# Performance work log

Hardware: AMD Instinct MI355X
Metric: run time of the kernel (lower is better)

## Reference

```python
import jax, jax.numpy as jnp
import numpy as np

V, E, H = 39, 512, 256  # vocab, emb_size, hidden_size (hard-coded in VQVAE)
B, T = 512, 128


def _p(key, shape, scale=0.05):
    return scale * jax.random.normal(key, shape, dtype=jnp.float32)


def setup_inputs() -> dict:
    key = jax.random.key(0)
    ks = jax.random.split(key, 24)
    inp = {}
    inp["input"] = jax.random.randint(ks[0], (B, T), 0, V)
    inp["src_emb_table"] = _p(ks[1], (V, E))
    inp["trg_emb_table"] = _p(ks[2], (V, E))
    # encoder bidirectional GRU (input E, hidden H), PyTorch layout (3H, in)/(3H, H)
    inp["enc_Wih_f"] = _p(ks[3], (3 * H, E)); inp["enc_Whh_f"] = _p(ks[4], (3 * H, H))
    inp["enc_bih_f"] = _p(ks[5], (3 * H,)); inp["enc_bhh_f"] = _p(ks[6], (3 * H,))
    inp["enc_Wih_b"] = _p(ks[7], (3 * H, E)); inp["enc_Whh_b"] = _p(ks[8], (3 * H, H))
    inp["enc_bih_b"] = _p(ks[9], (3 * H,)); inp["enc_bhh_b"] = _p(ks[10], (3 * H,))
    # bridge: Linear(2H -> H, bias=True)
    inp["bridge_W"] = _p(ks[11], (H, 2 * H)); inp["bridge_b"] = _p(ks[12], (H,))
    # Bahdanau attention: key (2H->H), query (H->H), energy (H->1), all bias-free
    inp["attn_Wk"] = _p(ks[13], (H, 2 * H))
    inp["attn_Wq"] = _p(ks[14], (H, H))
    inp["attn_We"] = _p(ks[15], (1, H))
    # decoder GRU (input E + 2H = 1024, hidden H)
    inp["dec_Wih"] = _p(ks[16], (3 * H, E + 2 * H)); inp["dec_Whh"] = _p(ks[17], (3 * H, H))
    inp["dec_bih"] = _p(ks[18], (3 * H,)); inp["dec_bhh"] = _p(ks[19], (3 * H,))
    # pre_output: Linear(H + 2H + E = 1280 -> H, bias=False)
    inp["pre_W"] = _p(ks[20], (H, H + 2 * H + E))
    # generator: Linear(H -> V, bias=False)
    inp["gen_W"] = _p(ks[21], (V, H))
    return inp


def gru_cell(x, h, Wih, Whh, bih, bhh):
    """PyTorch GRU cell: gates ordered [r, z, n]."""
    gi = x @ Wih.T + bih
    gh = h @ Whh.T + bhh
    ir, iz, inn = jnp.split(gi, 3, axis=-1)
    hr, hz, hn = jnp.split(gh, 3, axis=-1)
    r = jax.nn.sigmoid(ir + hr)
    z = jax.nn.sigmoid(iz + hz)
    n = jnp.tanh(inn + r * hn)
    return (1.0 - z) * n + z * h


def reference(input, src_emb_table, trg_emb_table,
              enc_Wih_f, enc_Whh_f, enc_bih_f, enc_bhh_f,
              enc_Wih_b, enc_Whh_b, enc_bih_b, enc_bhh_b,
              bridge_W, bridge_b, attn_Wk, attn_Wq, attn_We,
              dec_Wih, dec_Whh, dec_bih, dec_bhh, pre_W, gen_W):
    Bv, Tv = input.shape
    src_mask = input != 0                       # (B, T)
    trg = input[:, :-1]
    trg_y = input[:, 1:]

    # ---- Encoder: bidirectional GRU over full length (lengths == T) ----
    x = src_emb_table[input]                    # (B, T, E)
    xs = jnp.swapaxes(x, 0, 1)                  # (T, B, E)
    h0 = jnp.zeros((Bv, H), x.dtype)

    def step_f(h, xt):
        hn = gru_cell(xt, h, enc_Wih_f, enc_Whh_f, enc_bih_f, enc_bhh_f)
        return hn, hn

    def step_b(h, xt):
        hn = gru_cell(xt, h, enc_Wih_b, enc_Whh_b, enc_bih_b, enc_bhh_b)
        return hn, hn

    hf, out_f = jax.lax.scan(step_f, h0, xs)
    hb, out_b = jax.lax.scan(step_b, h0, xs[::-1])
    out_b = out_b[::-1]
    enc_out = jnp.swapaxes(jnp.concatenate([out_f, out_b], -1), 0, 1)  # (B, T, 2H)
    enc_final = jnp.concatenate([hf, hb], -1)                          # (B, 2H)

    # ---- Decoder init + precomputed attention keys ----
    hidden = jnp.tanh(enc_final @ bridge_W.T + bridge_b)               # (B, H)
    proj_key = enc_out @ attn_Wk.T                                     # (B, T, H)

    te = jnp.swapaxes(trg_emb_table[trg], 0, 1)                        # (T-1, B, E)
    neg = jnp.finfo(x.dtype).min

    def dec_step(h, prev_embed):
        q = h @ attn_Wq.T                                              # (B, H)
        e = jnp.tanh(q[:, None, :] + proj_key) @ attn_We[0]            # (B, T)
        e = jnp.where(src_mask, e, neg)
        a = jax.nn.softmax(e, axis=-1)                                 # (B, T)
        ctx = jnp.einsum('bt,btd->bd', a, enc_out)                     # (B, 2H)
        hn = gru_cell(jnp.concatenate([prev_embed, ctx], -1), h,
                      dec_Wih, dec_Whh, dec_bih, dec_bhh)              # (B, H)
        # dropout p=0.2 is identity in eval mode
        pre = jnp.concatenate([prev_embed, hn, ctx], -1) @ pre_W.T     # (B, H)
        return hn, pre

    _, pres = jax.lax.scan(dec_step, hidden, te)                       # (T-1, B, H)

    # ---- Generator + NLL loss (sum, ignore_index=0) ----
    logp = jax.nn.log_softmax(pres @ gen_W.T, axis=-1)                 # (T-1, B, V)
    ty = jnp.swapaxes(trg_y, 0, 1)                                     # (T-1, B)
    nll = -jnp.take_along_axis(logp, ty[..., None], axis=-1)[..., 0]
    loss = jnp.sum(jnp.where(ty != 0, nll, 0.0))
    return loss
```

## Files before the change

kernel.cpp:

```cpp
#include <hip/hip_runtime.h>

#define BB 512
#define TT 128
#define EE 512
#define HH 256
#define VV 39
#define H3 768
#define H2 512
#define TM1 127
#define NEGF (-3.402823466e38f)

typedef unsigned short u16;
typedef unsigned int u32;
typedef __attribute__((ext_vector_type(8))) short s16x8;
typedef __attribute__((ext_vector_type(4))) float f32x4;
typedef __attribute__((ext_vector_type(2))) unsigned int u32x2;
typedef __attribute__((ext_vector_type(4))) unsigned int u32x4;

__device__ __forceinline__ float b2f(u16 u){ u32 x=((u32)u)<<16; return __uint_as_float(x); }
__device__ __forceinline__ u16 f2b(float f){ u32 x=__float_as_uint(f); u32 r=(x+0x7fffu+((x>>16)&1u))>>16; return (u16)r; }
__device__ __forceinline__ float sigm(float x){ return 1.f/(1.f+__expf(-x)); }
__device__ __forceinline__ float tanh1(float x){ float t=__expf(2.f*x); return 1.f-2.f/(t+1.f); }
__device__ __forceinline__ float bfl(u32 u){ return __uint_as_float(u<<16); }
__device__ __forceinline__ float bfh(u32 u){ return __uint_as_float(u & 0xffff0000u); }

#define MFMA __builtin_amdgcn_mfma_f32_16x16x32_bf16

__device__ __forceinline__ u32 aload(const u32* p){
  return __hip_atomic_load(p, __ATOMIC_RELAXED, __HIP_MEMORY_SCOPE_AGENT);
}
__device__ __forceinline__ void astore(u32* p, u32 v){
  __hip_atomic_store(p, v, __ATOMIC_RELAXED, __HIP_MEMORY_SCOPE_AGENT);
}
#define QF(g) ((g)*16)

__global__ __launch_bounds__(256) void k_tables(
    const float* __restrict__ src_emb, const float* __restrict__ trg_emb,
    const float* __restrict__ Wih_f, const float* __restrict__ bih_f,
    const float* __restrict__ Wih_b, const float* __restrict__ bih_b,
    const float* __restrict__ dec_Wih, const float* __restrict__ dec_bih,
    const float* __restrict__ pre_W,
    float* __restrict__ tab_gi_f, float* __restrict__ tab_gi_b,
    float* __restrict__ tab_dec, float* __restrict__ tab_pre)
{
  int v = blockIdx.x;
  int y = blockIdx.y;
  int tid = threadIdx.x;
  if (y < 9){
    int seg = y/3, part = y%3;
    int n = part*256 + tid;
    const float* emb; const float* W; const float* bias; float* out; int ldw;
    if (seg==0){ emb=src_emb; W=Wih_f; bias=bih_f; out=tab_gi_f; ldw=EE; }
    else if (seg==1){ emb=src_emb; W=Wih_b; bias=bih_b; out=tab_gi_b; ldw=EE; }
    else { emb=trg_emb; W=dec_Wih; bias=dec_bih; out=tab_dec; ldw=EE+H2; }
    float acc = bias[n];
    const float* er = emb + (size_t)v*EE;
    const float* wr = W + (size_t)n*ldw;
    for (int k=0;k<EE;k++) acc += er[k]*wr[k];
    out[(size_t)v*H3 + n] = acc;
  } else {
    int n = tid;
    float acc = 0.f;
    const float* er = trg_emb + (size_t)v*EE;
    const float* wr = pre_W + (size_t)n*1280;
    for (int k=0;k<EE;k++) acc += er[k]*wr[k];
    tab_pre[(size_t)v*HH + n] = acc;
  }
}

__global__ __launch_bounds__(256) void k_cvt_all(
    const float* __restrict__ eWhh_f, const float* __restrict__ eWhh_b,
    const float* __restrict__ dWhh, const float* __restrict__ dWih,
    const float* __restrict__ Wk, const float* __restrict__ Wq,
    const float* __restrict__ preW, const float* __restrict__ genW,
    u16* __restrict__ o1, u16* __restrict__ o2, u16* __restrict__ o3,
    u16* __restrict__ o4, u16* __restrict__ o5, u16* __restrict__ o6,
    u16* __restrict__ o7, u16* __restrict__ o8, u16* __restrict__ o9)
{
  int idx = blockIdx.x*256 + threadIdx.x;
  const float* src; u16* dst; int cols, ld, off, rel;
  if      (idx <  196608){ rel=idx;          src=eWhh_f; dst=o1; cols=256; ld=256;  off=0;   }
  else if (idx <  393216){ rel=idx-196608;   src=eWhh_b; dst=o2; cols=256; ld=256;  off=0;   }
  else if (idx <  589824){ rel=idx-393216;   src=dWhh;   dst=o3; cols=256; ld=256;  off=0;   }
  else if (idx <  983040){ rel=idx-589824;   src=dWih;   dst=o4; cols=512; ld=1024; off=512; }
  else if (idx < 1114112){ rel=idx-983040;   src=Wk;     dst=o5; cols=512; ld=512;  off=0;   }
  else if (idx < 1179648){ rel=idx-1114112;  src=Wq;     dst=o6; cols=256; ld=256;  off=0;   }
  else if (idx < 1245184){ rel=idx-1179648;  src=preW;   dst=o7; cols=256; ld=1280; off=512; }
  else if (idx < 1376256){ rel=idx-1245184;  src=preW;   dst=o8; cols=512; ld=1280; off=768; }
  else if (idx < 1392640){
    rel=idx-1376256; int r=rel>>8, c2=rel&255;
    o9[rel] = (r<VV)? f2b(genW[(size_t)r*HH + c2]) : (u16)0;
    return;
  }
  else return;
  int r = rel/cols, c2 = rel - r*cols;
  dst[rel] = f2b(src[(size_t)r*ld + off + c2]);
}

__global__ __launch_bounds__(512) void k_enc_all(const int* __restrict__ input,
    const u16* __restrict__ wb_f, const u16* __restrict__ wb_b,
    const float* __restrict__ bhh_f, const float* __restrict__ bhh_b,
    const float* __restrict__ tab_f, const float* __restrict__ tab_b,
    float* __restrict__ h_f, float* __restrict__ h_b, u16* __restrict__ enc_out)
{
  __shared__ float gh[8][772];
  __shared__ u16 hs[16][264];
  int bx = blockIdx.x;
  int dirb = bx>>6, mt = bx&63;
  int m0 = mt*8;
  int tid = threadIdx.x;
  const float* tab = dirb? tab_b : tab_f;
  const float* bhh = dirb? bhh_b : bhh_f;
  const u16* Wb = dirb? wb_b : wb_f;
  int c = tid & 255, rh = tid>>8;
  float b_r=bhh[c], b_z=bhh[c+256], b_n=bhh[c+512];
  float hreg[4];
  #pragma unroll
  for (int r=0;r<4;r++) hreg[r]=0.f;
  int wv = tid>>6, lane = tid&63, l15 = lane&15, kg=(lane>>4)*8;
  int n0w = wv*96;
  float* hOut = dirb? h_b : h_f;
  { u16* z = &hs[0][0]; for (int e=tid; e<16*264; e+=512) z[e]=0; }
  __syncthreads();

  for (int s=1; s<=TT; s++){
    int tcol = dirb? (TT-s) : (s-1);
    #pragma unroll
    for (int r=0;r<4;r++){
      int row = rh*4 + r;
      int b = m0 + row;
      int tok = input[b*TT + tcol];
      const float* tg = tab + (size_t)tok*H3;
      float g0=0.f, g1=0.f, g2=0.f;
      if (s>1){ g0=gh[row][c]; g1=gh[row][c+256]; g2=gh[row][c+512]; }
      float rg = sigm(tg[c]     + g0 + b_r);
      float zg = sigm(tg[c+256] + g1 + b_z);
      float ng = tanh1(tg[c+512] + rg*(g2 + b_n));
      float hv = (1.f-zg)*ng + zg*hreg[r];
      hreg[r] = hv;
      u16 hb = f2b(hv);
      hs[row][c] = hb;
      enc_out[((size_t)b*TT + tcol)*H2 + (size_t)dirb*HH + c] = hb;
    }
    if (s==TT){
      #pragma unroll
      for (int r=0;r<4;r++)
        hOut[(size_t)(m0+rh*4+r)*HH + c] = hreg[r];
      break;
    }
    __syncthreads();
    f32x4 acc[6];
    #pragma unroll
    for (int nt=0;nt<6;nt++) acc[nt]=(f32x4){0.f,0.f,0.f,0.f};
    const u16* ar0 = &hs[l15][0];
    s16x8 bcur[6], bnext[6];
    #pragma unroll
    for (int nt=0;nt<6;nt++)
      bcur[nt] = *(const s16x8*)(Wb + (size_t)(n0w+nt*16+l15)*HH + kg);
    #pragma unroll
    for (int ko=0;ko<256;ko+=32){
      if (ko<224){
        #pragma unroll
        for (int nt=0;nt<6;nt++)
          bnext[nt] = *(const s16x8*)(Wb + (size_t)(n0w+nt*16+l15)*HH + ko+32 + kg);
      }
      s16x8 a0 = *(const s16x8*)(ar0 + ko + kg);
      #pragma unroll
      for (int nt=0;nt<6;nt++)
        acc[nt] = MFMA(a0, bcur[nt], acc[nt], 0,0,0);
      #pragma unroll
      for (int nt=0;nt<6;nt++) bcur[nt]=bnext[nt];
    }
    int q4 = (lane>>4)*4;
    if (q4 < 8){
      #pragma unroll
      for (int nt=0;nt<6;nt++){
        int col = n0w + nt*16 + l15;
        #pragma unroll
        for (int j=0;j<4;j++)
          gh[q4 + j][col] = acc[nt][j];
      }
    }
    __syncthreads();
  }
}

__global__ __launch_bounds__(256) void k_proj(const u16* __restrict__ enc,
    const u16* __restrict__ W, u16* __restrict__ out, int nTot)
{
  int m0 = blockIdx.x*64;
  int tid = threadIdx.x, wv = tid>>6, lane = tid&63;
  int l15 = lane&15, kg = (lane>>4)*8;
  int n0 = blockIdx.y*256 + wv*64;
  f32x4 acc[4][4];
  #pragma unroll
  for (int rt=0;rt<4;rt++)
    #pragma unroll
    for (int nt=0;nt<4;nt++) acc[rt][nt] = (f32x4){0.f,0.f,0.f,0.f};
  for (int ko=0; ko<512; ko+=32){
    s16x8 a[4], b[4];
    #pragma unroll
    for (int rt=0;rt<4;rt++) a[rt] = *(const s16x8*)(enc + (size_t)(m0+rt*16+l15)*H2 + ko + kg);
    #pragma unroll
    for (int nt=0;nt<4;nt++) b[nt] = *(const s16x8*)(W + (size_t)(n0+nt*16+l15)*H2 + ko + kg);
    #pragma unroll
    for (int rt=0;rt<4;rt++)
      #pragma unroll
      for (int nt=0;nt<4;nt++)
        acc[rt][nt] = MFMA(a[rt], b[nt], acc[rt][nt], 0,0,0);
  }
  #pragma unroll
  for (int rt=0;rt<4;rt++){
    int rbase = m0 + rt*16 + (lane>>4)*4;
    #pragma unroll
    for (int nt=0;nt<4;nt++){
      int col = n0 + nt*16 + l15;
      #pragma unroll
      for (int j=0;j<4;j++)
        out[(size_t)(rbase+j)*nTot + col] = f2b(acc[rt][nt][j]);
    }
  }
}

__global__ __launch_bounds__(256) void k_bridge(const float* __restrict__ h_f,
    const float* __restrict__ h_b, const float* __restrict__ bw,
    const float* __restrict__ bb, float* __restrict__ hst)
{
  __shared__ float As[32][68];
  __shared__ float Ws[32][68];
  int n0=blockIdx.x*64, m0=blockIdx.y*64, tid=threadIdx.x;
  int ar=tid>>2, ak=(tid&3)*8;
  int rt=tid>>4, ct=tid&15;
  float acc[4][4];
  #pragma unroll
  for (int j=0;j<4;j++){
    #pragma unroll
    for (int l=0;l<4;l++) acc[j][l]=0.f;
  }
  for (int ko=0;ko<512;ko+=32){
    int k0=ko+ak;
    const float* asrc = (k0<256)? (h_f + (size_t)(m0+ar)*HH + k0)
                                : (h_b + (size_t)(m0+ar)*HH + (k0-256));
    float4 a0=*(const float4*)asrc, a1=*(const float4*)(asrc+4);
    const float* wsrc = bw + (size_t)(n0+ar)*H2 + k0;
    float4 w0=*(const float4*)wsrc, w1=*(const float4*)(wsrc+4);
    __syncthreads();
    As[ak+0][ar]=a0.x; As[ak+1][ar]=a0.y; As[ak+2][ar]=a0.z; As[ak+3][ar]=a0.w;
    As[ak+4][ar]=a1.x; As[ak+5][ar]=a1.y; As[ak+6][ar]=a1.z; As[ak+7][ar]=a1.w;
    Ws[ak+0][ar]=w0.x; Ws[ak+1][ar]=w0.y; Ws[ak+2][ar]=w0.z; Ws[ak+3][ar]=w0.w;
    Ws[ak+4][ar]=w1.x; Ws[ak+5][ar]=w1.y; Ws[ak+6][ar]=w1.z; Ws[ak+7][ar]=w1.w;
    __syncthreads();
    #pragma unroll
    for (int kk=0;kk<32;kk++){
      float4 a=*(const float4*)&As[kk][rt*4];
      float4 w=*(const float4*)&Ws[kk][ct*4];
      float a4[4]={a.x,a.y,a.z,a.w};
      float w4[4]={w.x,w.y,w.z,w.w};
      #pragma unroll
      for (int j=0;j<4;j++){
        #pragma unroll
        for (int l=0;l<4;l++) acc[j][l]+=a4[j]*w4[l];
      }
    }
  }
  #pragma unroll
  for (int j=0;j<4;j++){
    int row=m0+rt*4+j;
    #pragma unroll
    for (int l=0;l<4;l++){
      int col=n0+ct*4+l;
      hst[(size_t)row*HH+col]=tanh1(acc[j][l]+bb[col]);
    }
  }
}

__global__ __launch_bounds__(256) void k_boot(
    const float* __restrict__ hst, const u16* __restrict__ whh,
    const u16* __restrict__ wq, float* __restrict__ ghg,
    float* __restrict__ qg, float* __restrict__ nll)
{
  __shared__ u16 hsb[16][264];
  int bx=blockIdx.x, tid=threadIdx.x;
  int wv=tid>>6, lane=tid&63, l15=lane&15, kg=(lane>>4)*8;
  int b0=bx*16;
  {
    int c=tid;
    for (int r=0;r<16;r++) hsb[r][c] = f2b(hst[(size_t)(b0+r)*HH + c]);
  }
  if (tid<16) nll[b0+tid] = 0.f;
  __syncthreads();
  int rr = (lane>>4)*4;
  for (int nt=0;nt<12;nt++){
    int n0 = wv*192 + nt*16;
    f32x4 acc = (f32x4){0.f,0.f,0.f,0.f};
    for (int ko=0;ko<256;ko+=32){
      s16x8 a = *(const s16x8*)&hsb[l15][ko+kg];
      s16x8 bf = *(const s16x8*)(whh + (size_t)(n0+l15)*HH + ko + kg);
      acc = MFMA(a, bf, acc, 0,0,0);
    }
    #pragma unroll
    for (int jr=0;jr<4;jr++)
      ghg[(size_t)(b0+rr+jr)*H3 + n0 + l15] = acc[jr];
  }
  #pragma unroll
  for (int nt=0;nt<4;nt++){
    int n0 = wv*64 + nt*16;
    f32x4 acc = (f32x4){0.f,0.f,0.f,0.f};
    for (int ko=0;ko<256;ko+=32){
      s16x8 a = *(const s16x8*)&hsb[l15][ko+kg];
      s16x8 bf = *(const s16x8*)(wq + (size_t)(n0+l15)*HH + ko + kg);
      acc = MFMA(a, bf, acc, 0,0,0);
    }
    #pragma unroll
    for (int jr=0;jr<4;jr++)
      qg[(size_t)(b0+rr+jr)*HH + n0 + l15] = acc[jr];
  }
}

__global__ __launch_bounds__(512,4) void k_step(int L,
    const int* __restrict__ input,
    const float* __restrict__ tab_dec, const float* __restrict__ tab_pre,
    const float* __restrict__ bhh, const float* __restrict__ We,
    const u16* __restrict__ whh, const u16* __restrict__ wq,
    const u16* __restrict__ wph, const u16* __restrict__ wgen,
    const u16* __restrict__ pk, const u16* __restrict__ eih,
    const u16* __restrict__ epc,
    float* __restrict__ hst, u32* __restrict__ qgu, float* __restrict__ ghg,
    u16* __restrict__ gicW, const u16* __restrict__ gicR,
    u16* __restrict__ pcW, const u16* __restrict__ pcR,
    float* __restrict__ nll, u32* __restrict__ fl)
{
  __shared__ __align__(16) char smem[54400];
  u16 (*gicL)[776] = (u16(*)[776])smem;
  u16 (*pcl)[264]  = (u16(*)[264])(smem+24832);
  u16 (*hsb)[264]  = (u16(*)[264])(smem+33280);
  u16 (*preb)[264] = (u16(*)[264])(smem+41728);
  float (*lgt)[64] = (float(*)[64])(smem+50176);
  int* stokL       = (int*)(smem+54272);
  float* aL  = (float*)smem;
  int* stok  = (int*)(smem+512);
  float* qS  = (float*)(smem+1024);
  float (*pG)[768] = (float(*)[768])(smem+2048);
  float (*pP)[256] = (float(*)[256])(smem+26624);

  int bx=blockIdx.x, tid=threadIdx.x;
  int wv=tid>>6, lane=tid&63, l15=lane&15, kg=(lane>>4)*8;

  if (bx < 32 && L > 0){
    int s = L-1;
    int b0 = bx*16;
    int rr = (lane>>4)*4;
    float b_r, b_z, b_n;
    { int c=tid&255; b_r=bhh[c]; b_z=bhh[c+256]; b_n=bhh[c+512]; }
    for (int idx=tid; idx<1536; idx+=512){
      int r=idx/96, cc=(idx%96)*8;
      *(u32x4*)&gicL[r][cc] = *(const u32x4*)(gicR + (size_t)(b0+r)*H3 + cc);
    }
    { int r=tid>>5, cc=(tid&31)*8;
      *(u32x4*)&pcl[r][cc] = *(const u32x4*)(pcR + (size_t)(b0+r)*HH + cc); }
    if (tid<16) stokL[tid] = input[(b0+tid)*TT + s];
    __syncthreads();
    {
      int c = tid&255, rh = tid>>8;
      for (int r=rh*8; r<rh*8+8; r++){
        int bb = b0+r;
        const float* tg = tab_dec + (size_t)stokL[r]*H3;
        const float* gr = ghg + (size_t)bb*H3;
        float rg = sigm(tg[c]     + b2f(gicL[r][c])     + gr[c]     + b_r);
        float zg = sigm(tg[c+256] + b2f(gicL[r][c+256]) + gr[c+256] + b_z);
        float ng = tanh1(tg[c+512] + b2f(gicL[r][c+512]) + rg*(gr[c+512] + b_n));
        float hv = (1.f-zg)*ng + zg*hst[(size_t)bb*HH + c];
        hst[(size_t)bb*HH + c] = hv;
        hsb[r][c] = f2b(hv);
      }
    }
    __syncthreads();
    {
      f32x4 accq[2];
      accq[0]=(f32x4){0.f,0.f,0.f,0.f}; accq[1]=(f32x4){0.f,0.f,0.f,0.f};
      #pragma unroll
      for (int ko=0;ko<256;ko+=32){
        s16x8 bq0 = *(const s16x8*)(wq + (size_t)(wv*32+l15)*HH + ko + kg);
        s16x8 bq1 = *(const s16x8*)(wq + (size_t)(wv*32+16+l15)*HH + ko + kg);
        s16x8 a = *(const s16x8*)&hsb[l15][ko+kg];
        accq[0] = MFMA(a,bq0,accq[0],0,0,0);
        accq[1] = MFMA(a,bq1,accq[1],0,0,0);
      }
      #pragma unroll
      for (int nt=0;nt<2;nt++)
        #pragma unroll
        for (int jr=0;jr<4;jr++)
          astore(qgu + (size_t)(b0+rr+jr)*HH + wv*32+nt*16+l15,
                 __float_as_uint(accq[nt][jr]));
    }
    __syncthreads();
    if (tid==0) astore(&fl[QF(bx)], (u32)L);
    {
      f32x4 acc6[6];
      #pragma unroll
      for (int nt=0;nt<6;nt++) acc6[nt]=(f32x4){0.f,0.f,0.f,0.f};
      #pragma unroll
      for (int ko=0;ko<256;ko+=32){
        s16x8 b6[6];
        #pragma unroll
        for (int nt=0;nt<6;nt++)
          b6[nt] = *(const s16x8*)(whh + (size_t)(wv*96+nt*16+l15)*HH + ko + kg);
        s16x8 a = *(const s16x8*)&hsb[l15][ko+kg];
        #pragma unroll
        for (int nt=0;nt<6;nt++) acc6[nt]=MFMA(a,b6[nt],acc6[nt],0,0,0);
      }
      #pragma unroll
      for (int nt=0;nt<6;nt++)
        #pragma unroll
        for (int jr=0;jr<4;jr++)
          ghg[(size_t)(b0+rr+jr)*H3 + wv*96+nt*16+l15] = acc6[nt][jr];
    }
    {
      f32x4 accp[2];
      accp[0]=(f32x4){0.f,0.f,0.f,0.f}; accp[1]=(f32x4){0.f,0.f,0.f,0.f};
      #pragma unroll
      for (int ko=0;ko<256;ko+=32){
        s16x8 bp0 = *(const s16x8*)(wph + (size_t)(wv*32+l15)*HH + ko + kg);
        s16x8 bp1 = *(const s16x8*)(wph + (size_t)(wv*32+16+l15)*HH + ko + kg);
        s16x8 a = *(const s16x8*)&hsb[l15][ko+kg];
        accp[0] = MFMA(a,bp0,accp[0],0,0,0);
        accp[1] = MFMA(a,bp1,accp[1],0,0,0);
      }
      #pragma unroll
      for (int nt=0;nt<2;nt++)
        #pragma unroll
        for (int jr=0;jr<4;jr++){
          int r = rr+jr, col = wv*32+nt*16+l15;
          float pv = accp[nt][jr] + b2f(pcl[r][col]) + tab_pre[(size_t)stokL[r]*HH + col];
          preb[r][col] = f2b(pv);
        }
    }
    __syncthreads();
    if (wv<4){
      int n0 = wv*16;
      f32x4 acc = (f32x4){0.f,0.f,0.f,0.f};
      for (int ko=0;ko<256;ko+=32){
        s16x8 a = *(const s16x8*)&preb[l15][ko+kg];
        s16x8 bf = *(const s16x8*)(wgen + (size_t)(n0+l15)*HH + ko + kg);
        acc = MFMA(a,bf,acc,0,0,0);
      }
      #pragma unroll
      for (int jr=0;jr<4;jr++) lgt[rr+jr][n0+l15] = acc[jr];
    }
    __syncthreads();
    {
      int r = wv*4 + (lane>>4);
      if (r < 16){
        float v0 = lgt[r][l15];
        float v1 = lgt[r][l15+16];
        float v2 = (l15<7)? lgt[r][l15+32] : NEGF;
        float m = fmaxf(fmaxf(v0,v1),v2);
        #pragma unroll
        for (int off=8; off; off>>=1) m = fmaxf(m, __shfl_xor(m,off));
        float pe = __expf(v0-m) + __expf(v1-m) + ((l15<7)? __expf(v2-m) : 0.f);
        #pragma unroll
        for (int off=8; off; off>>=1) pe += __shfl_xor(pe,off);
        if (l15==0){
          int ty = input[(b0+r)*TT + s+1];
          if (ty != 0) nll[b0+r] += m + __logf(pe) - lgt[r][ty];
        }
      }
    }
    __syncthreads();
  }

  if (L < TM1){
    int r2 = bx;
    int g2 = r2>>4;
    int l32 = lane&31;
    if (tid < TT) stok[tid] = input[r2*TT + tid];
    const u16* pkb = pk + (size_t)r2*TT*HH + l32*8;
    s16x8 kv[8];
    #pragma unroll
    for (int it=0; it<8; it++){
      int t = wv*16 + it*2 + (lane>>5);
      kv[it] = *(const s16x8*)(pkb + (size_t)t*HH);
    }
    float4 w0 = *(const float4*)(We + l32*8);
    float4 w1 = *(const float4*)(We + l32*8 + 4);
    __syncthreads();
    if (L > 0){
      if (tid==0){
        while (aload(&fl[QF(g2)]) < (u32)L) __builtin_amdgcn_s_sleep(1);
      }
      __syncthreads();
    }
    if (tid < 256) qS[tid] = __uint_as_float(aload(qgu + (size_t)r2*HH + tid));
    __syncthreads();
    float4 q0 = *(const float4*)&qS[l32*8];
    float4 q1 = *(const float4*)&qS[l32*8 + 4];
    #pragma unroll
    for (int it=0; it<8; it++){
      int t = wv*16 + it*2 + (lane>>5);
      s16x8 k8 = kv[it];
      float sE = tanh1(q0.x + b2f((u16)k8[0]))*w0.x
               + tanh1(q0.y + b2f((u16)k8[1]))*w0.y
               + tanh1(q0.z + b2f((u16)k8[2]))*w0.z
               + tanh1(q0.w + b2f((u16)k8[3]))*w0.w
               + tanh1(q1.x + b2f((u16)k8[4]))*w1.x
               + tanh1(q1.y + b2f((u16)k8[5]))*w1.y
               + tanh1(q1.z + b2f((u16)k8[6]))*w1.z
               + tanh1(q1.w + b2f((u16)k8[7]))*w1.w;
      #pragma unroll
      for (int off=16; off; off>>=1) sE += __shfl_xor(sE, off);
      if (l32==0) aL[t] = stok[t] ? sE : NEGF;
    }
    __syncthreads();
    if (wv==0){
      float v0 = aL[lane], v1 = aL[64+lane];
      float m = fmaxf(v0,v1);
      #pragma unroll
      for (int off=32; off; off>>=1) m = fmaxf(m, __shfl_xor(m,off));
      float p0 = __expf(v0-m), p1 = __expf(v1-m);
      float sS = p0+p1;
      #pragma unroll
      for (int off=32; off; off>>=1) sS += __shfl_xor(sS,off);
      float inv = 1.f/sS;
      aL[lane] = p0*inv; aL[64+lane] = p1*inv;
    }
    __syncthreads();
    {
      float gA[8], gB[4], pA[4];
      #pragma unroll
      for (int e=0;e<8;e++) gA[e]=0.f;
      #pragma unroll
      for (int e=0;e<4;e++){ gB[e]=0.f; pA[e]=0.f; }
      const u16* ei = eih + (size_t)r2*TT*H3;
      const u16* ep = epc + (size_t)r2*TT*HH;
      int t0 = wv*16;
      #pragma unroll 4
      for (int tt=0; tt<16; tt++){
        int t = t0+tt;
        float a = aL[t];
        u32x4 v0 = *(const u32x4*)(ei + (size_t)t*H3 + lane*8);
        u32x2 v1 = *(const u32x2*)(ei + (size_t)t*H3 + 512 + lane*4);
        u32x2 v2 = *(const u32x2*)(ep + (size_t)t*HH + lane*4);
        gA[0]+=a*bfl(v0.x); gA[1]+=a*bfh(v0.x);
        gA[2]+=a*bfl(v0.y); gA[3]+=a*bfh(v0.y);
        gA[4]+=a*bfl(v0.z); gA[5]+=a*bfh(v0.z);
        gA[6]+=a*bfl(v0.w); gA[7]+=a*bfh(v0.w);
        gB[0]+=a*bfl(v1.x); gB[1]+=a*bfh(v1.x);
        gB[2]+=a*bfl(v1.y); gB[3]+=a*bfh(v1.y);
        pA[0]+=a*bfl(v2.x); pA[1]+=a*bfh(v2.x);
        pA[2]+=a*bfl(v2.y); pA[3]+=a*bfh(v2.y);
      }
      #pragma unroll
      for (int e=0;e<8;e++) pG[wv][lane*8+e] = gA[e];
      #pragma unroll
      for (int e=0;e<4;e++) pG[wv][512+lane*4+e] = gB[e];
      #pragma unroll
      for (int e=0;e<4;e++) pP[wv][lane*4+e] = pA[e];
    }
    __syncthreads();
    {
      float sG = 0.f;
      #pragma unroll
      for (int w=0;w<8;w++) sG += pG[w][tid];
      gicW[(size_t)r2*H3 + tid] = f2b(sG);
      if (tid < 256){
        float sH = 0.f;
        #pragma unroll
        for (int w=0;w<8;w++) sH += pG[w][512+tid];
        gicW[(size_t)r2*H3 + 512 + tid] = f2b(sH);
      } else {
        int d = tid-256;
        float sP = 0.f;
        #pragma unroll
        for (int w=0;w<8;w++) sP += pP[w][d];
        pcW[(size_t)r2*HH + d] = f2b(sP);
      }
    }
  }
}

__global__ __launch_bounds__(256) void k_loss(const float* __restrict__ nll,
                                              float* __restrict__ out)
{
  __shared__ float sm[256];
  int tid=threadIdx.x;
  float s = nll[tid] + nll[tid+256];
  sm[tid]=s; __syncthreads();
  for (int off=128; off; off>>=1){
    if (tid<off) sm[tid]+=sm[tid+off];
    __syncthreads();
  }
  if (tid==0) out[0]=sm[0];
}

extern "C" void kernel_launch(void* const* d_in, const int* in_sizes, int n_in,
                              void* d_out, int out_size, void* d_ws, size_t ws_size,
                              hipStream_t stream)
{
  const int*   input    = (const int*)  d_in[0];
  const float* src_emb  = (const float*)d_in[1];
  const float* trg_emb  = (const float*)d_in[2];
  const float* eWih_f   = (const float*)d_in[3];
  const float* eWhh_f   = (const float*)d_in[4];
  const float* ebih_f   = (const float*)d_in[5];
  const float* ebhh_f   = (const float*)d_in[6];
  const float* eWih_b   = (const float*)d_in[7];
  const float* eWhh_b   = (const float*)d_in[8];
  const float* ebih_b   = (const float*)d_in[9];
  const float* ebhh_b   = (const float*)d_in[10];
  const float* bridge_W = (const float*)d_in[11];
  const float* bridge_b = (const float*)d_in[12];
  const float* attn_Wk  = (const float*)d_in[13];
  const float* attn_Wq  = (const float*)d_in[14];
  const float* attn_We  = (const float*)d_in[15];
  const float* dec_Wih  = (const float*)d_in[16];
  const float* dec_Whh  = (const float*)d_in[17];
  const float* dec_bih  = (const float*)d_in[18];
  const float* dec_bhh  = (const float*)d_in[19];
  const float* pre_W    = (const float*)d_in[20];
  const float* gen_W    = (const float*)d_in[21];

  float* F = (float*)d_ws;
  size_t o=0;
  u32* fl         = (u32*)(F+o); o+=2048;
  float* tab_gi_f = F+o; o+=(size_t)VV*H3;
  float* tab_gi_b = F+o; o+=(size_t)VV*H3;
  float* tab_dec  = F+o; o+=(size_t)VV*H3;
  float* tab_pre  = F+o; o+=(size_t)VV*HH;
  float* h_f      = F+o; o+=(size_t)BB*HH;
  float* h_b      = F+o; o+=(size_t)BB*HH;
  float* hst      = F+o; o+=(size_t)BB*HH;
  float* qg       = F+o; o+=(size_t)BB*HH;
  float* ghg      = F+o; o+=(size_t)BB*H3;
  float* nll      = F+o; o+=(size_t)BB;
  u16* U = (u16*)(F+o);
  size_t uo=0;
  u16* enc_out = U+uo; uo+=(size_t)BB*TT*H2;
  u16* pk      = U+uo; uo+=(size_t)BB*TT*HH;
  u16* eih     = U+uo; uo+=(size_t)BB*TT*H3;
  u16* epc     = U+uo; uo+=(size_t)BB*TT*HH;
  u16* gic0    = U+uo; uo+=(size_t)BB*H3;
  u16* gic1    = U+uo; uo+=(size_t)BB*H3;
  u16* pc0     = U+uo; uo+=(size_t)BB*HH;
  u16* pc1     = U+uo; uo+=(size_t)BB*HH;
  u16* wb_ehh_f= U+uo; uo+=(size_t)H3*HH;
  u16* wb_ehh_b= U+uo; uo+=(size_t)H3*HH;
  u16* wb_dhh  = U+uo; uo+=(size_t)H3*HH;
  u16* wb_dih  = U+uo; uo+=(size_t)H3*H2;
  u16* wb_wk   = U+uo; uo+=(size_t)HH*H2;
  u16* wb_wq   = U+uo; uo+=(size_t)HH*HH;
  u16* wb_ph   = U+uo; uo+=(size_t)HH*HH;
  u16* wb_pc   = U+uo; uo+=(size_t)HH*H2;
  u16* wb_gen  = U+uo; uo+=(size_t)64*HH;

  dim3 blk(256,1,1);
  k_tables<<<dim3(VV,10),blk,0,stream>>>(src_emb,trg_emb,eWih_f,ebih_f,eWih_b,ebih_b,
                                         dec_Wih,dec_bih,pre_W,
                                         tab_gi_f,tab_gi_b,tab_dec,tab_pre);
  k_cvt_all<<<dim3(5440),blk,0,stream>>>(eWhh_f,eWhh_b,dec_Whh,dec_Wih,attn_Wk,attn_Wq,pre_W,gen_W,
                                         wb_ehh_f,wb_ehh_b,wb_dhh,wb_dih,wb_wk,wb_wq,
                                         wb_ph,wb_pc,wb_gen);
  k_enc_all<<<dim3(128),dim3(512),0,stream>>>(input,wb_ehh_f,wb_ehh_b,ebhh_f,ebhh_b,
                                              tab_gi_f,tab_gi_b,h_f,h_b,enc_out);
  k_proj<<<dim3(1024,1),blk,0,stream>>>(enc_out,wb_wk,pk,HH);
  k_proj<<<dim3(1024,3),blk,0,stream>>>(enc_out,wb_dih,eih,H3);
  k_proj<<<dim3(1024,1),blk,0,stream>>>(enc_out,wb_pc,epc,HH);
  k_bridge<<<dim3(4,8),blk,0,stream>>>(h_f,h_b,bridge_W,bridge_b,hst);
  k_boot<<<dim3(32),blk,0,stream>>>(hst,wb_dhh,wb_wq,ghg,qg,nll);
  hipMemsetAsync(fl, 0, 8192, stream);

  for (int L=0; L<=TM1; L++){
    u16* gw = (L&1)? gic1 : gic0;
    u16* gr = (L&1)? gic0 : gic1;
    u16* pw = (L&1)? pc1 : pc0;
    u16* pr = (L&1)? pc0 : pc1;
    k_step<<<dim3(512),dim3(512),0,stream>>>(L,input,tab_dec,tab_pre,dec_bhh,attn_We,
                                             wb_dhh,wb_wq,wb_ph,wb_gen,
                                             pk,eih,epc,hst,(u32*)qg,ghg,
                                             gw,gr,pw,pr,nll,fl);
  }
  k_loss<<<dim3(1),blk,0,stream>>>(nll,(float*)d_out);
}
```

Baseline: 8.778 ms.

## Fuse decoder steps into one persistent kernel with flag-based inter-block sync

Replaces the 128 per-step k_step launches with a single persistent kernel of 256 blocks that loops over all decoder steps. Blocks exchange gate and pre-output contributions through double-buffered global buffers, using atomic flags and spin-waits in place of kernel boundaries. Each attention block now handles two batch rows instead of one, and the encoder is split into 256 blocks of 4 rows to raise parallelism. This removes launch overhead and implicit grid barriers, but adds spin-wait latency and relies on all 256 blocks being co-resident to avoid deadlock.

```diff
diff --git a/kernel.cpp b/kernel.cpp
--- a/kernel.cpp
+++ b/kernel.cpp
@@ -33,6 +33,7 @@
   __hip_atomic_store(p, v, __ATOMIC_RELAXED, __HIP_MEMORY_SCOPE_AGENT);
 }
 #define QF(g) ((g)*16)
+#define GF(b) (512 + (b)*16)
 
 __global__ __launch_bounds__(256) void k_tables(
     const float* __restrict__ src_emb, const float* __restrict__ trg_emb,
@@ -103,20 +104,19 @@
     const float* __restrict__ tab_f, const float* __restrict__ tab_b,
     float* __restrict__ h_f, float* __restrict__ h_b, u16* __restrict__ enc_out)
 {
-  __shared__ float gh[8][772];
+  __shared__ float gh[4][772];
   __shared__ u16 hs[16][264];
   int bx = blockIdx.x;
-  int dirb = bx>>6, mt = bx&63;
-  int m0 = mt*8;
+  int dirb = bx>>7, mt = bx&127;
+  int m0 = mt*4;
   int tid = threadIdx.x;
   const float* tab = dirb? tab_b : tab_f;
   const float* bhh = dirb? bhh_b : bhh_f;
   const u16* Wb = dirb? wb_b : wb_f;
   int c = tid & 255, rh = tid>>8;
   float b_r=bhh[c], b_z=bhh[c+256], b_n=bhh[c+512];
-  float hreg[4];
-  #pragma unroll
-  for (int r=0;r<4;r++) hreg[r]=0.f;
+  float hreg[2];
+  hreg[0]=0.f; hreg[1]=0.f;
   int wv = tid>>6, lane = tid&63, l15 = lane&15, kg=(lane>>4)*8;
   int n0w = wv*96;
   float* hOut = dirb? h_b : h_f;
@@ -126,8 +126,8 @@
   for (int s=1; s<=TT; s++){
     int tcol = dirb? (TT-s) : (s-1);
     #pragma unroll
-    for (int r=0;r<4;r++){
-      int row = rh*4 + r;
+    for (int r=0;r<2;r++){
+      int row = rh*2 + r;
       int b = m0 + row;
       int tok = input[b*TT + tcol];
       const float* tg = tab + (size_t)tok*H3;
@@ -144,8 +144,8 @@
     }
     if (s==TT){
       #pragma unroll
-      for (int r=0;r<4;r++)
-        hOut[(size_t)(m0+rh*4+r)*HH + c] = hreg[r];
+      for (int r=0;r<2;r++)
+        hOut[(size_t)(m0+rh*2+r)*HH + c] = hreg[r];
       break;
     }
     __syncthreads();
@@ -172,13 +172,13 @@
       for (int nt=0;nt<6;nt++) bcur[nt]=bnext[nt];
     }
     int q4 = (lane>>4)*4;
-    if (q4 < 8){
+    if (q4 == 0){
       #pragma unroll
       for (int nt=0;nt<6;nt++){
         int col = n0w + nt*16 + l15;
         #pragma unroll
         for (int j=0;j<4;j++)
-          gh[q4 + j][col] = acc[nt][j];
+          gh[j][col] = acc[nt][j];
       }
     }
     __syncthreads();
@@ -317,7 +317,7 @@
   }
 }
 
-__global__ __launch_bounds__(512,4) void k_step(int L,
+__global__ __launch_bounds__(512,2) void k_dec_p(
     const int* __restrict__ input,
     const float* __restrict__ tab_dec, const float* __restrict__ tab_pre,
     const float* __restrict__ bhh, const float* __restrict__ We,
@@ -326,8 +326,7 @@
     const u16* __restrict__ pk, const u16* __restrict__ eih,
     const u16* __restrict__ epc,
     float* __restrict__ hst, u32* __restrict__ qgu, float* __restrict__ ghg,
-    u16* __restrict__ gicW, const u16* __restrict__ gicR,
-    u16* __restrict__ pcW, const u16* __restrict__ pcR,
+    u32* __restrict__ gp0, u32* __restrict__ gp1,
     float* __restrict__ nll, u32* __restrict__ fl)
 {
   __shared__ __align__(16) char smem[54400];
@@ -336,244 +335,252 @@
   u16 (*hsb)[264]  = (u16(*)[264])(smem+33280);
   u16 (*preb)[264] = (u16(*)[264])(smem+41728);
   float (*lgt)[64] = (float(*)[64])(smem+50176);
-  int* stokL       = (int*)(smem+54272);
   float* aL  = (float*)smem;
-  int* stok  = (int*)(smem+512);
   float* qS  = (float*)(smem+1024);
-  float (*pG)[768] = (float(*)[768])(smem+2048);
-  float (*pP)[256] = (float(*)[256])(smem+26624);
+  float (*pG)[768] = (float(*)[768])(smem+4096);
+  float (*pP)[256] = (float(*)[256])(smem+28672);
+  __shared__ int stokA[256];
+  __shared__ int stokG[16];
 
   int bx=blockIdx.x, tid=threadIdx.x;
   int wv=tid>>6, lane=tid&63, l15=lane&15, kg=(lane>>4)*8;
-
-  if (bx < 32 && L > 0){
-    int s = L-1;
-    int b0 = bx*16;
-    int rr = (lane>>4)*4;
-    float b_r, b_z, b_n;
-    { int c=tid&255; b_r=bhh[c]; b_z=bhh[c+256]; b_n=bhh[c+512]; }
-    for (int idx=tid; idx<1536; idx+=512){
-      int r=idx/96, cc=(idx%96)*8;
-      *(u32x4*)&gicL[r][cc] = *(const u32x4*)(gicR + (size_t)(b0+r)*H3 + cc);
-    }
-    { int r=tid>>5, cc=(tid&31)*8;
-      *(u32x4*)&pcl[r][cc] = *(const u32x4*)(pcR + (size_t)(b0+r)*HH + cc); }
-    if (tid<16) stokL[tid] = input[(b0+tid)*TT + s];
-    __syncthreads();
-    {
-      int c = tid&255, rh = tid>>8;
-      for (int r=rh*8; r<rh*8+8; r++){
-        int bb = b0+r;
-        const float* tg = tab_dec + (size_t)stokL[r]*H3;
-        const float* gr = ghg + (size_t)bb*H3;
-        float rg = sigm(tg[c]     + b2f(gicL[r][c])     + gr[c]     + b_r);
-        float zg = sigm(tg[c+256] + b2f(gicL[r][c+256]) + gr[c+256] + b_z);
-        float ng = tanh1(tg[c+512] + b2f(gicL[r][c+512]) + rg*(gr[c+512] + b_n));
-        float hv = (1.f-zg)*ng + zg*hst[(size_t)bb*HH + c];
-        hst[(size_t)bb*HH + c] = hv;
-        hsb[r][c] = f2b(hv);
-      }
-    }
-    __syncthreads();
-    {
-      f32x4 accq[2];
-      accq[0]=(f32x4){0.f,0.f,0.f,0.f}; accq[1]=(f32x4){0.f,0.f,0.f,0.f};
-      #pragma unroll
-      for (int ko=0;ko<256;ko+=32){
-        s16x8 bq0 = *(const s16x8*)(wq + (size_t)(wv*32+l15)*HH + ko + kg);
-        s16x8 bq1 = *(const s16x8*)(wq + (size_t)(wv*32+16+l15)*HH + ko + kg);
-        s16x8 a = *(const s16x8*)&hsb[l15][ko+kg];
-        accq[0] = MFMA(a,bq0,accq[0],0,0,0);
-        accq[1] = MFMA(a,bq1,accq[1],0,0,0);
-      }
-      #pragma unroll
-      for (int nt=0;nt<2;nt++)
-        #pragma unroll
-        for (int jr=0;jr<4;jr++)
-          astore(qgu + (size_t)(b0+rr+jr)*HH + wv*32+nt*16+l15,
-                 __float_as_uint(accq[nt][jr]));
-    }
-    __syncthreads();
-    if (tid==0) astore(&fl[QF(bx)], (u32)L);
-    {
-      f32x4 acc6[6];
-      #pragma unroll
-      for (int nt=0;nt<6;nt++) acc6[nt]=(f32x4){0.f,0.f,0.f,0.f};
-      #pragma unroll
-      for (int ko=0;ko<256;ko+=32){
-        s16x8 b6[6];
+  int rr = (lane>>4)*4;
+  int b0 = bx*16;
+  int rowA = bx*2;
+  int g2 = bx>>3;
+  int l32 = lane&31;
+  float b_r, b_z, b_n;
+  { int c=tid&255; b_r=bhh[c]; b_z=bhh[c+256]; b_n=bhh[c+512]; }
+  float4 w0 = *(const float4*)(We + l32*8);
+  float4 w1 = *(const float4*)(We + l32*8 + 4);
+  if (tid<256) stokA[tid] = input[(rowA + (tid>>7))*TT + (tid&127)];
+  __syncthreads();
+
+  for (int L=0; L<=TM1; L++){
+    if (bx < 32 && L > 0){
+      int s = L-1;
+      const u32* gpR = ((L-1)&1)? gp1 : gp0;
+      if (tid<8){
+        while (aload(&fl[GF(bx*8+tid)]) < (u32)L) __builtin_amdgcn_s_sleep(1);
+      }
+      if (tid<16) stokG[tid] = input[(b0+tid)*TT + s];
+      __syncthreads();
+      for (int idx=tid; idx<8192; idx+=512){
+        int r = idx>>9, k = idx&511;
+        u32 v = aload(gpR + (size_t)(b0+r)*512 + k);
+        if (k<384) *(u32*)&gicL[r][2*k] = v;
+        else       *(u32*)&pcl[r][2*(k-384)] = v;
+      }
+      __syncthreads();
+      {
+        int c = tid&255, rh = tid>>8;
+        for (int r=rh*8; r<rh*8+8; r++){
+          int bb = b0+r;
+          const float* tg = tab_dec + (size_t)stokG[r]*H3;
+          const float* gr = ghg + (size_t)bb*H3;
+          float rg = sigm(tg[c]     + b2f(gicL[r][c])     + gr[c]     + b_r);
+          float zg = sigm(tg[c+256] + b2f(gicL[r][c+256]) + gr[c+256] + b_z);
+          float ng = tanh1(tg[c+512] + b2f(gicL[r][c+512]) + rg*(gr[c+512] + b_n));
+          float hv = (1.f-zg)*ng + zg*hst[(size_t)bb*HH + c];
+          hst[(size_t)bb*HH + c] = hv;
+          hsb[r][c] = f2b(hv);
+        }
+      }
+      __syncthreads();
+      {
+        f32x4 accq[2];
+        accq[0]=(f32x4){0.f,0.f,0.f,0.f}; accq[1]=(f32x4){0.f,0.f,0.f,0.f};
+        #pragma unroll
+        for (int ko=0;ko<256;ko+=32){
+          s16x8 bq0 = *(const s16x8*)(wq + (size_t)(wv*32+l15)*HH + ko + kg);
+          s16x8 bq1 = *(const s16x8*)(wq + (size_t)(wv*32+16+l15)*HH + ko + kg);
+          s16x8 a = *(const s16x8*)&hsb[l15][ko+kg];
+          accq[0] = MFMA(a,bq0,accq[0],0,0,0);
+          accq[1] = MFMA(a,bq1,accq[1],0,0,0);
+        }
+        #pragma unroll
+        for (int nt=0;nt<2;nt++)
+          #pragma unroll
+          for (int jr=0;jr<4;jr++)
+            astore(qgu + (size_t)(b0+rr+jr)*HH + wv*32+nt*16+l15,
+                   __float_as_uint(accq[nt][jr]));
+      }
+      __syncthreads();
+      if (tid==0) astore(&fl[QF(bx)], (u32)L);
+      {
+        f32x4 acc6[6];
+        #pragma unroll
+        for (int nt=0;nt<6;nt++) acc6[nt]=(f32x4){0.f,0.f,0.f,0.f};
+        #pragma unroll
+        for (int ko=0;ko<256;ko+=32){
+          s16x8 b6[6];
+          #pragma unroll
+          for (int nt=0;nt<6;nt++)
+            b6[nt] = *(const s16x8*)(whh + (size_t)(wv*96+nt*16+l15)*HH + ko + kg);
+          s16x8 a = *(const s16x8*)&hsb[l15][ko+kg];
+          #pragma unroll
+          for (int nt=0;nt<6;nt++) acc6[nt]=MFMA(a,b6[nt],acc6[nt],0,0,0);
+        }
         #pragma unroll
         for (int nt=0;nt<6;nt++)
-          b6[nt] = *(const s16x8*)(whh + (size_t)(wv*96+nt*16+l15)*HH + ko + kg);
-        s16x8 a = *(const s16x8*)&hsb[l15][ko+kg];
-        #pragma unroll
-        for (int nt=0;nt<6;nt++) acc6[nt]=MFMA(a,b6[nt],acc6[nt],0,0,0);
-      }
-      #pragma unroll
-      for (int nt=0;nt<6;nt++)
-        #pragma unroll
-        for (int jr=0;jr<4;jr++)
-          ghg[(size_t)(b0+rr+jr)*H3 + wv*96+nt*16+l15] = acc6[nt][jr];
-    }
-    {
-      f32x4 accp[2];
-      accp[0]=(f32x4){0.f,0.f,0.f,0.f}; accp[1]=(f32x4){0.f,0.f,0.f,0.f};
-      #pragma unroll
-      for (int ko=0;ko<256;ko+=32){
-        s16x8 bp0 = *(const s16x8*)(wph + (size_t)(wv*32+l15)*HH + ko + kg);
-        s16x8 bp1 = *(const s16x8*)(wph + (size_t)(wv*32+16+l15)*HH + ko + kg);
-        s16x8 a = *(const s16x8*)&hsb[l15][ko+kg];
-        accp[0] = MFMA(a,bp0,accp[0],0,0,0);
-        accp[1] = MFMA(a,bp1,accp[1],0,0,0);
-      }
-      #pragma unroll
-      for (int nt=0;nt<2;nt++)
-        #pragma unroll
-        for (int jr=0;jr<4;jr++){
-          int r = rr+jr, col = wv*32+nt*16+l15;
-          float pv = accp[nt][jr] + b2f(pcl[r][col]) + tab_pre[(size_t)stokL[r]*HH + col];
-          preb[r][col] = f2b(pv);
-        }
-    }
-    __syncthreads();
-    if (wv<4){
-      int n0 = wv*16;
-      f32x4 acc = (f32x4){0.f,0.f,0.f,0.f};
-      for (int ko=0;ko<256;ko+=32){
-        s16x8 a = *(const s16x8*)&preb[l15][ko+kg];
-        s16x8 bf = *(const s16x8*)(wgen + (size_t)(n0+l15)*HH + ko + kg);
-        acc = MFMA(a,bf,acc,0,0,0);
-      }
-      #pragma unroll
-      for (int jr=0;jr<4;jr++) lgt[rr+jr][n0+l15] = acc[jr];
-    }
-    __syncthreads();
-    {
-      int r = wv*4 + (lane>>4);
-      if (r < 16){
-        float v0 = lgt[r][l15];
-        float v1 = lgt[r][l15+16];
-        float v2 = (l15<7)? lgt[r][l15+32] : NEGF;
-        float m = fmaxf(fmaxf(v0,v1),v2);
-        #pragma unroll
-        for (int off=8; off; off>>=1) m = fmaxf(m, __shfl_xor(m,off));
-        float pe = __expf(v0-m) + __expf(v1-m) + ((l15<7)? __expf(v2-m) : 0.f);
-        #pragma unroll
-        for (int off=8; off; off>>=1) pe += __shfl_xor(pe,off);
-        if (l15==0){
-          int ty = input[(b0+r)*TT + s+1];
-          if (ty != 0) nll[b0+r] += m + __logf(pe) - lgt[r][ty];
-        }
-      }
-    }
-    __syncthreads();
-  }
-
-  if (L < TM1){
-    int r2 = bx;
-    int g2 = r2>>4;
-    int l32 = lane&31;
-    if (tid < TT) stok[tid] = input[r2*TT + tid];
-    const u16* pkb = pk + (size_t)r2*TT*HH + l32*8;
-    s16x8 kv[8];
-    #pragma unroll
-    for (int it=0; it<8; it++){
-      int t = wv*16 + it*2 + (lane>>5);
-      kv[it] = *(const s16x8*)(pkb + (size_t)t*HH);
-    }
-    float4 w0 = *(const float4*)(We + l32*8);
-    float4 w1 = *(const float4*)(We + l32*8 + 4);
-    __syncthreads();
-    if (L > 0){
-      if (tid==0){
-        while (aload(&fl[QF(g2)]) < (u32)L) __builtin_amdgcn_s_sleep(1);
-      }
-      __syncthreads();
-    }
-    if (tid < 256) qS[tid] = __uint_as_float(aload(qgu + (size_t)r2*HH + tid));
-    __syncthreads();
-    float4 q0 = *(const float4*)&qS[l32*8];
-    float4 q1 = *(const float4*)&qS[l32*8 + 4];
-    #pragma unroll
-    for (int it=0; it<8; it++){
-      int t = wv*16 + it*2 + (lane>>5);
-      s16x8 k8 = kv[it];
-      float sE = tanh1(q0.x + b2f((u16)k8[0]))*w0.x
-               + tanh1(q0.y + b2f((u16)k8[1]))*w0.y
-               + tanh1(q0.z + b2f((u16)k8[2]))*w0.z
-               + tanh1(q0.w + b2f((u16)k8[3]))*w0.w
-               + tanh1(q1.x + b2f((u16)k8[4]))*w1.x
-               + tanh1(q1.y + b2f((u16)k8[5]))*w1.y
-               + tanh1(q1.z + b2f((u16)k8[6]))*w1.z
-               + tanh1(q1.w + b2f((u16)k8[7]))*w1.w;
-      #pragma unroll
-      for (int off=16; off; off>>=1) sE += __shfl_xor(sE, off);
-      if (l32==0) aL[t] = stok[t] ? sE : NEGF;
-    }
-    __syncthreads();
-    if (wv==0){
-      float v0 = aL[lane], v1 = aL[64+lane];
-      float m = fmaxf(v0,v1);
-      #pragma unroll
-      for (int off=32; off; off>>=1) m = fmaxf(m, __shfl_xor(m,off));
-      float p0 = __expf(v0-m), p1 = __expf(v1-m);
-      float sS = p0+p1;
-      #pragma unroll
-      for (int off=32; off; off>>=1) sS += __shfl_xor(sS,off);
-      float inv = 1.f/sS;
-      aL[lane] = p0*inv; aL[64+lane] = p1*inv;
-    }
-    __syncthreads();
-    {
-      float gA[8], gB[4], pA[4];
-      #pragma unroll
-      for (int e=0;e<8;e++) gA[e]=0.f;
-      #pragma unroll
-      for (int e=0;e<4;e++){ gB[e]=0.f; pA[e]=0.f; }
-      const u16* ei = eih + (size_t)r2*TT*H3;
-      const u16* ep = epc + (size_t)r2*TT*HH;
-      int t0 = wv*16;
-      #pragma unroll 4
-      for (int tt=0; tt<16; tt++){
-        int t = t0+tt;
-        float a = aL[t];
-        u32x4 v0 = *(const u32x4*)(ei + (size_t)t*H3 + lane*8);
-        u32x2 v1 = *(const u32x2*)(ei + (size_t)t*H3 + 512 + lane*4);
-        u32x2 v2 = *(const u32x2*)(ep + (size_t)t*HH + lane*4);
-        gA[0]+=a*bfl(v0.x); gA[1]+=a*bfh(v0.x);
-        gA[2]+=a*bfl(v0.y); gA[3]+=a*bfh(v0.y);
-        gA[4]+=a*bfl(v0.z); gA[5]+=a*bfh(v0.z);
-        gA[6]+=a*bfl(v0.w); gA[7]+=a*bfh(v0.w);
-        gB[0]+=a*bfl(v1.x); gB[1]+=a*bfh(v1.x);
-        gB[2]+=a*bfl(v1.y); gB[3]+=a*bfh(v1.y);
-        pA[0]+=a*bfl(v2.x); pA[1]+=a*bfh(v2.x);
-        pA[2]+=a*bfl(v2.y); pA[3]+=a*bfh(v2.y);
-      }
-      #pragma unroll
-      for (int e=0;e<8;e++) pG[wv][lane*8+e] = gA[e];
-      #pragma unroll
-      for (int e=0;e<4;e++) pG[wv][512+lane*4+e] = gB[e];
-      #pragma unroll
-      for (int e=0;e<4;e++) pP[wv][lane*4+e] = pA[e];
-    }
-    __syncthreads();
-    {
-      float sG = 0.f;
-      #pragma unroll
-      for (int w=0;w<8;w++) sG += pG[w][tid];
-      gicW[(size_t)r2*H3 + tid] = f2b(sG);
-      if (tid < 256){
-        float sH = 0.f;
-        #pragma unroll
-        for (int w=0;w<8;w++) sH += pG[w][512+tid];
-        gicW[(size_t)r2*H3 + 512 + tid] = f2b(sH);
-      } else {
-        int d = tid-256;
-        float sP = 0.f;
-        #pragma unroll
-        for (int w=0;w<8;w++) sP += pP[w][d];
-        pcW[(size_t)r2*HH + d] = f2b(sP);
-      }
+          #pragma unroll
+          for (int jr=0;jr<4;jr++)
+            ghg[(size_t)(b0+rr+jr)*H3 + wv*96+nt*16+l15] = acc6[nt][jr];
+      }
+      {
+        f32x4 accp[2];
+        accp[0]=(f32x4){0.f,0.f,0.f,0.f}; accp[1]=(f32x4){0.f,0.f,0.f,0.f};
+        #pragma unroll
+        for (int ko=0;ko<256;ko+=32){
+          s16x8 bp0 = *(const s16x8*)(wph + (size_t)(wv*32+l15)*HH + ko + kg);
+          s16x8 bp1 = *(const s16x8*)(wph + (size_t)(wv*32+16+l15)*HH + ko + kg);
+          s16x8 a = *(const s16x8*)&hsb[l15][ko+kg];
+          accp[0] = MFMA(a,bp0,accp[0],0,0,0);
+          accp[1] = MFMA(a,bp1,accp[1],0,0,0);
+        }
+        #pragma unroll
+        for (int nt=0;nt<2;nt++)
+          #pragma unroll
+          for (int jr=0;jr<4;jr++){
+            int r = rr+jr, col = wv*32+nt*16+l15;
+            float pv = accp[nt][jr] + b2f(pcl[r][col]) + tab_pre[(size_t)stokG[r]*HH + col];
+            preb[r][col] = f2b(pv);
+          }
+      }
+      __syncthreads();
+      if (wv<4){
+        int n0 = wv*16;
+        f32x4 acc = (f32x4){0.f,0.f,0.f,0.f};
+        for (int ko=0;ko<256;ko+=32){
+          s16x8 a = *(const s16x8*)&preb[l15][ko+kg];
+          s16x8 bf = *(const s16x8*)(wgen + (size_t)(n0+l15)*HH + ko + kg);
+          acc = MFMA(a,bf,acc,0,0,0);
+        }
+        #pragma unroll
+        for (int jr=0;jr<4;jr++) lgt[rr+jr][n0+l15] = acc[jr];
+      }
+      __syncthreads();
+      {
+        int r = wv*4 + (lane>>4);
+        if (r < 16){
+          float v0 = lgt[r][l15];
+          float v1 = lgt[r][l15+16];
+          float v2 = (l15<7)? lgt[r][l15+32] : NEGF;
+          float m = fmaxf(fmaxf(v0,v1),v2);
+          #pragma unroll
+          for (int off=8; off; off>>=1) m = fmaxf(m, __shfl_xor(m,off));
+          float pe = __expf(v0-m) + __expf(v1-m) + ((l15<7)? __expf(v2-m) : 0.f);
+          #pragma unroll
+          for (int off=8; off; off>>=1) pe += __shfl_xor(pe,off);
+          if (l15==0){
+            int ty = input[(b0+r)*TT + s+1];
+            if (ty != 0) nll[b0+r] += m + __logf(pe) - lgt[r][ty];
+          }
+        }
+      }
+      __syncthreads();
+    }
+
+    if (L < TM1){
+      u32* gpW = (L&1)? gp1 : gp0;
+      if (L > 0){
+        if (tid==0){
+          while (aload(&fl[QF(g2)]) < (u32)L) __builtin_amdgcn_s_sleep(1);
+        }
+        __syncthreads();
+      }
+      qS[tid] = __uint_as_float(aload(qgu + (size_t)rowA*HH + tid));
+      __syncthreads();
+      for (int rp=0; rp<2; rp++){
+        int row = rowA + rp;
+        const u16* pkb = pk + (size_t)row*TT*HH + l32*8;
+        s16x8 kv[8];
+        #pragma unroll
+        for (int it=0; it<8; it++){
+          int t = wv*16 + it*2 + (lane>>5);
+          kv[it] = *(const s16x8*)(pkb + (size_t)t*HH);
+        }
+        float4 q0 = *(const float4*)&qS[rp*256 + l32*8];
+        float4 q1 = *(const float4*)&qS[rp*256 + l32*8 + 4];
+        #pragma unroll
+        for (int it=0; it<8; it++){
+          int t = wv*16 + it*2 + (lane>>5);
+          s16x8 k8 = kv[it];
+          float sE = tanh1(q0.x + b2f((u16)k8[0]))*w0.x
+                   + tanh1(q0.y + b2f((u16)k8[1]))*w0.y
+                   + tanh1(q0.z + b2f((u16)k8[2]))*w0.z
+                   + tanh1(q0.w + b2f((u16)k8[3]))*w0.w
+                   + tanh1(q1.x + b2f((u16)k8[4]))*w1.x
+                   + tanh1(q1.y + b2f((u16)k8[5]))*w1.y
+                   + tanh1(q1.z + b2f((u16)k8[6]))*w1.z
+                   + tanh1(q1.w + b2f((u16)k8[7]))*w1.w;
+          #pragma unroll
+          for (int off=16; off; off>>=1) sE += __shfl_xor(sE, off);
+          if (l32==0) aL[t] = stokA[rp*128+t] ? sE : NEGF;
+        }
+        __syncthreads();
+        if (wv==0){
+          float v0 = aL[lane], v1 = aL[64+lane];
+          float m = fmaxf(v0,v1);
+          #pragma unroll
+          for (int off=32; off; off>>=1) m = fmaxf(m, __shfl_xor(m,off));
+          float p0 = __expf(v0-m), p1 = __expf(v1-m);
+          float sS = p0+p1;
+          #pragma unroll
+          for (int off=32; off; off>>=1) sS += __shfl_xor(sS,off);
+          float inv = 1.f/sS;
+          aL[lane] = p0*inv; aL[64+lane] = p1*inv;
+        }
+        __syncthreads();
+        {
+          float gA[8], gB[4], pA[4];
+          #pragma unroll
+          for (int e=0;e<8;e++) gA[e]=0.f;
+          #pragma unroll
+          for (int e=0;e<4;e++){ gB[e]=0.f; pA[e]=0.f; }
+          const u16* ei = eih + (size_t)row*TT*H3;
+          const u16* ep = epc + (size_t)row*TT*HH;
+          int t0 = wv*16;
+          #pragma unroll 4
+          for (int tt=0; tt<16; tt++){
+            int t = t0+tt;
+            float a = aL[t];
+            u32x4 v0 = *(const u32x4*)(ei + (size_t)t*H3 + lane*8);
+            u32x2 v1 = *(const u32x2*)(ei + (size_t)t*H3 + 512 + lane*4);
+            u32x2 v2 = *(const u32x2*)(ep + (size_t)t*HH + lane*4);
+            gA[0]+=a*bfl(v0.x); gA[1]+=a*bfh(v0.x);
+            gA[2]+=a*bfl(v0.y); gA[3]+=a*bfh(v0.y);
+            gA[4]+=a*bfl(v0.z); gA[5]+=a*bfh(v0.z);
+            gA[6]+=a*bfl(v0.w); gA[7]+=a*bfh(v0.w);
+            gB[0]+=a*bfl(v1.x); gB[1]+=a*bfh(v1.x);
+            gB[2]+=a*bfl(v1.y); gB[3]+=a*bfh(v1.y);
+            pA[0]+=a*bfl(v2.x); pA[1]+=a*bfh(v2.x);
+            pA[2]+=a*bfl(v2.y); pA[3]+=a*bfh(v2.y);
+          }
+          #pragma unroll
+          for (int e=0;e<8;e++) pG[wv][lane*8+e] = gA[e];
+          #pragma unroll
+          for (int e=0;e<4;e++) pG[wv][512+lane*4+e] = gB[e];
+          #pragma unroll
+          for (int e=0;e<4;e++) pP[wv][lane*4+e] = pA[e];
+        }
+        __syncthreads();
+        {
+          float lo=0.f, hi=0.f;
+          if (tid<384){
+            #pragma unroll
+            for (int w=0;w<8;w++){ lo += pG[w][2*tid]; hi += pG[w][2*tid+1]; }
+          } else {
+            int d = tid-384;
+            #pragma unroll
+            for (int w=0;w<8;w++){ lo += pP[w][2*d]; hi += pP[w][2*d+1]; }
+          }
+          u32 v = (u32)f2b(lo) | ((u32)f2b(hi)<<16);
+          astore(gpW + (size_t)row*512 + tid, v);
+        }
+        __syncthreads();
+      }
+      if (tid==0) astore(&fl[GF(bx)], (u32)(L+1));
     }
   }
 }
@@ -621,7 +628,7 @@
 
   float* F = (float*)d_ws;
   size_t o=0;
-  u32* fl         = (u32*)(F+o); o+=2048;
+  u32* fl         = (u32*)(F+o); o+=8192;
   float* tab_gi_f = F+o; o+=(size_t)VV*H3;
   float* tab_gi_b = F+o; o+=(size_t)VV*H3;
   float* tab_dec  = F+o; o+=(size_t)VV*H3;
@@ -632,16 +639,14 @@
   float* qg       = F+o; o+=(size_t)BB*HH;
   float* ghg      = F+o; o+=(size_t)BB*H3;
   float* nll      = F+o; o+=(size_t)BB;
+  u32* gp0        = (u32*)(F+o); o+=(size_t)BB*512;
+  u32* gp1        = (u32*)(F+o); o+=(size_t)BB*512;
   u16* U = (u16*)(F+o);
   size_t uo=0;
   u16* enc_out = U+uo; uo+=(size_t)BB*TT*H2;
   u16* pk      = U+uo; uo+=(size_t)BB*TT*HH;
   u16* eih     = U+uo; uo+=(size_t)BB*TT*H3;
   u16* epc     = U+uo; uo+=(size_t)BB*TT*HH;
-  u16* gic0    = U+uo; uo+=(size_t)BB*H3;
-  u16* gic1    = U+uo; uo+=(size_t)BB*H3;
-  u16* pc0     = U+uo; uo+=(size_t)BB*HH;
-  u16* pc1     = U+uo; uo+=(size_t)BB*HH;
   u16* wb_ehh_f= U+uo; uo+=(size_t)H3*HH;
   u16* wb_ehh_b= U+uo; uo+=(size_t)H3*HH;
   u16* wb_dhh  = U+uo; uo+=(size_t)H3*HH;
@@ -659,24 +664,17 @@
   k_cvt_all<<<dim3(5440),blk,0,stream>>>(eWhh_f,eWhh_b,dec_Whh,dec_Wih,attn_Wk,attn_Wq,pre_W,gen_W,
                                          wb_ehh_f,wb_ehh_b,wb_dhh,wb_dih,wb_wk,wb_wq,
                                          wb_ph,wb_pc,wb_gen);
-  k_enc_all<<<dim3(128),dim3(512),0,stream>>>(input,wb_ehh_f,wb_ehh_b,ebhh_f,ebhh_b,
+  k_enc_all<<<dim3(256),dim3(512),0,stream>>>(input,wb_ehh_f,wb_ehh_b,ebhh_f,ebhh_b,
                                               tab_gi_f,tab_gi_b,h_f,h_b,enc_out);
   k_proj<<<dim3(1024,1),blk,0,stream>>>(enc_out,wb_wk,pk,HH);
   k_proj<<<dim3(1024,3),blk,0,stream>>>(enc_out,wb_dih,eih,H3);
   k_proj<<<dim3(1024,1),blk,0,stream>>>(enc_out,wb_pc,epc,HH);
   k_bridge<<<dim3(4,8),blk,0,stream>>>(h_f,h_b,bridge_W,bridge_b,hst);
   k_boot<<<dim3(32),blk,0,stream>>>(hst,wb_dhh,wb_wq,ghg,qg,nll);
-  hipMemsetAsync(fl, 0, 8192, stream);
-
-  for (int L=0; L<=TM1; L++){
-    u16* gw = (L&1)? gic1 : gic0;
-    u16* gr = (L&1)? gic0 : gic1;
-    u16* pw = (L&1)? pc1 : pc0;
-    u16* pr = (L&1)? pc0 : pc1;
-    k_step<<<dim3(512),dim3(512),0,stream>>>(L,input,tab_dec,tab_pre,dec_bhh,attn_We,
-                                             wb_dhh,wb_wq,wb_ph,wb_gen,
-                                             pk,eih,epc,hst,(u32*)qg,ghg,
-                                             gw,gr,pw,pr,nll,fl);
-  }
+  hipMemsetAsync(fl, 0, 32768, stream);
+  k_dec_p<<<dim3(256),dim3(512),0,stream>>>(input,tab_dec,tab_pre,dec_bhh,attn_We,
+                                            wb_dhh,wb_wq,wb_ph,wb_gen,
+                                            pk,eih,epc,hst,(u32*)qg,ghg,
+                                            gp0,gp1,nll,fl);
   k_loss<<<dim3(1),blk,0,stream>>>(nll,(float*)d_out);
 }
```

Result: slower. 9.567 ms (+9.0%).
